# Performance work log

Measured on AMD Instinct MI355X. Metric: run time of the kernel, lower is better.

Reference implementation:

```python
import jax, jax.numpy as jnp
import numpy as np

B, C, S, HEADS, MLP = 8, 128, 32, 8, 512
EPS = 1e-5
SCALE = (C // HEADS) ** -0.5  # dim_head=16 -> 16**-0.5


def setup_inputs() -> dict:
    key = jax.random.key(0)
    ks = jax.random.split(key, 6)
    x = jax.random.normal(ks[0], (B, C, S, S, S), jnp.float32)
    qkv_w = jax.random.normal(ks[1], (3 * C, C), jnp.float32) * 0.02   # Conv3d 1x1x1, no bias
    proj_w = jax.random.normal(ks[2], (C, C), jnp.float32) * 0.02
    proj_b = jnp.zeros((C,), jnp.float32)
    ln1_w = jnp.ones((C, S, S, S), jnp.float32)
    ln1_b = jnp.zeros((C, S, S, S), jnp.float32)
    ln2_w = jnp.ones((C, S, S, S), jnp.float32)
    ln2_b = jnp.zeros((C, S, S, S), jnp.float32)
    mlp_w1 = jax.random.normal(ks[3], (MLP, C), jnp.float32) * 0.02
    mlp_b1 = jnp.zeros((MLP,), jnp.float32)
    mlp_w2 = jax.random.normal(ks[4], (C, MLP), jnp.float32) * 0.02
    mlp_b2 = jnp.zeros((C,), jnp.float32)
    return dict(x=x, qkv_w=qkv_w, proj_w=proj_w, proj_b=proj_b,
                ln1_w=ln1_w, ln1_b=ln1_b, ln2_w=ln2_w, ln2_b=ln2_b,
                mlp_w1=mlp_w1, mlp_b1=mlp_b1, mlp_w2=mlp_w2, mlp_b2=mlp_b2)


def _layernorm_full(x, w, b):
    # LayerNorm over (channel, D, H, W) per batch element, biased variance, eps=1e-5
    mu = jnp.mean(x, axis=(1, 2, 3, 4), keepdims=True)
    var = jnp.mean(jnp.square(x - mu), axis=(1, 2, 3, 4), keepdims=True)
    return (x - mu) * jax.lax.rsqrt(var + EPS) * w[None] + b[None]


def _block(x, qkv_w, proj_w, proj_b, ln1_w, ln1_b, ln2_w, ln2_b,
           mlp_w1, mlp_b1, mlp_w2, mlp_b2):
    b, c, d, h, w = x.shape
    n = d * h * w
    ch = c // HEADS
    xf = x.reshape(b, c, n)
    # 1x1x1 conv == per-voxel matmul over channels
    qkv = jnp.einsum('bcn,oc->bon', xf, qkv_w)                 # [b, 3c, n]
    q, k, v = jnp.split(qkv, 3, axis=1)
    q = q.reshape(b, HEADS, ch, n)
    k = k.reshape(b, HEADS, ch, n)
    v = v.reshape(b, HEADS, ch, n)
    # channel-channel attention: contraction over spatial tokens n
    attn = jax.nn.softmax(jnp.einsum('bhin,bhjn->bhij', q, k) * SCALE, axis=-1)
    out = jnp.einsum('bhij,bhjn->bhin', attn, v).reshape(b, c, n)
    out = jnp.einsum('bcn,oc->bon', out, proj_w) + proj_b[None, :, None]
    x1 = _layernorm_full(x + out.reshape(b, c, d, h, w), ln1_w, ln1_b)
    # MLP: conv1x1 -> exact GELU -> conv1x1
    x1f = x1.reshape(b, c, n)
    hid = jax.nn.gelu(jnp.einsum('bcn,oc->bon', x1f, mlp_w1) + mlp_b1[None, :, None],
                      approximate=False)
    m = jnp.einsum('bon,co->bcn', hid, mlp_w2) + mlp_b2[None, :, None]
    return _layernorm_full(x1 + m.reshape(b, c, d, h, w), ln2_w, ln2_b)


def reference(x, qkv_w, proj_w, proj_b, ln1_w, ln1_b, ln2_w, ln2_b,
              mlp_w1, mlp_b1, mlp_w2, mlp_b2):
    return _block(x, qkv_w, proj_w, proj_b, ln1_w, ln1_b, ln2_w, ln2_b,
                  mlp_w1, mlp_b1, mlp_w2, mlp_b2)
```

## Files before the change

kernel.cpp:

```cpp
#include <hip/hip_runtime.h>
#include <hip/hip_bf16.h>
#include <math.h>


#define N_SP 32768
typedef __hip_bfloat16 bf16;
static const size_t DS = (size_t)128 * N_SP;

typedef __attribute__((ext_vector_type(8))) short s8b;
typedef __attribute__((ext_vector_type(4))) float f4;
typedef __attribute__((ext_vector_type(4))) uint u4v;
typedef __attribute__((ext_vector_type(4))) ushort us4v;

__device__ __forceinline__ ushort f2b(float f) {
    __hip_bfloat16 h = __float2bfloat16(f);
    return *reinterpret_cast<ushort*>(&h);
}
__device__ __forceinline__ float b2f(ushort u) {
    unsigned v = ((unsigned)u) << 16;
    float f;
    __builtin_memcpy(&f, &v, 4);
    return f;
}
__device__ __forceinline__ float gelu_f(float h) {
    float u = 1.5957691216057308f * h * fmaf(0.044715f, h * h, 1.0f);
    float e = __expf(u);
    return h * (1.0f - __builtin_amdgcn_rcpf(e + 1.0f));
}
__device__ __forceinline__ int swz8(int n, int c0) {
    return n * 128 + (c0 ^ ((n & 15) << 3));
}
__device__ __forceinline__ int swz4(int n, int c0) {
    return n * 128 + (((c0 & 0x78) ^ ((n & 15) << 3)) | (c0 & 4));
}

__global__ __launch_bounds__(256) void k_transpose(const float* __restrict__ in,
                                                   float* __restrict__ out,
                                                   int R, int Ccols) {
    int idx = blockIdx.x * 256 + threadIdx.x;
    if (idx >= R * Ccols) return;
    int r = idx / Ccols, c = idx % Ccols;
    out[c * R + r] = in[idx];
}

__global__ __launch_bounds__(256) void k_cvt(const float* __restrict__ in,
                                             ushort* __restrict__ out, int n) {
    int i = blockIdx.x * 256 + threadIdx.x;
    if (i < n) out[i] = f2b(in[i]);
}

__global__ __launch_bounds__(256) void k_packln(const float* __restrict__ w,
                                                const float* __restrict__ b,
                                                uint* __restrict__ out) {
    __shared__ uint tile[64 * 128];
    const int n0 = blockIdx.x * 64;
    const int t = threadIdx.x;
    {
        const int c = t >> 1, nh = (t & 1) * 32;
        const float* wp = w + (size_t)c * N_SP + n0 + nh;
        const float* bp = b + (size_t)c * N_SP + n0 + nh;
#pragma unroll
        for (int g = 0; g < 8; ++g) {
            f4 wv = __builtin_nontemporal_load((const f4*)(wp + g * 4));
            f4 bv = __builtin_nontemporal_load((const f4*)(bp + g * 4));
            tile[(nh + g * 4 + 0) * 128 + c] = (uint)f2b(wv.x) | ((uint)f2b(bv.x) << 16);
            tile[(nh + g * 4 + 1) * 128 + c] = (uint)f2b(wv.y) | ((uint)f2b(bv.y) << 16);
            tile[(nh + g * 4 + 2) * 128 + c] = (uint)f2b(wv.z) | ((uint)f2b(bv.z) << 16);
            tile[(nh + g * 4 + 3) * 128 + c] = (uint)f2b(wv.w) | ((uint)f2b(bv.w) << 16);
        }
    }
    __syncthreads();
    uint* op = out + (size_t)n0 * 128;
#pragma unroll
    for (int g = 0; g < 8; ++g) {
        int idx = g * 256 + t;
        *(uint4*)(op + idx * 4) = *(const uint4*)&tile[idx * 4];
    }
}

__global__ __launch_bounds__(256, 4) void k_cov(const float* __restrict__ x,
                                                float* __restrict__ Gpart) {
    __shared__ ushort xs[128 * 136];
    const int kb = blockIdx.x, b = blockIdx.y;
    const int t = threadIdx.x;
    const int wave = t >> 6, lane = t & 63, q = lane >> 4, r = lane & 15;
    f4 acc[8][2];
#pragma unroll
    for (int m = 0; m < 8; ++m) { acc[m][0] = (f4){0,0,0,0}; acc[m][1] = (f4){0,0,0,0}; }
    for (int ch = 0; ch < 4; ++ch) {
        const int nbase = kb * 512 + ch * 128;
        __syncthreads();
        {
            const int nq = t & 31, cr = t >> 5;
            const float* xp = x + (size_t)b * DS + nbase + nq * 4;
#pragma unroll
            for (int half = 0; half < 2; ++half) {
                f4 xv[8];
#pragma unroll
                for (int cc = 0; cc < 8; ++cc)
                    xv[cc] = __builtin_nontemporal_load(
                        (const f4*)(xp + (size_t)(cr * 16 + half * 8 + cc) * N_SP));
#pragma unroll
                for (int cc = 0; cc < 8; ++cc) {
                    int c = cr * 16 + half * 8 + cc;
                    ushort4 pk;
                    pk.x = f2b(xv[cc].x); pk.y = f2b(xv[cc].y);
                    pk.z = f2b(xv[cc].z); pk.w = f2b(xv[cc].w);
                    *(ushort4*)&xs[c * 136 + nq * 4] = pk;
                }
            }
        }
        __syncthreads();
        for (int kk = 0; kk < 4; ++kk) {
            const int c0 = kk * 32 + q * 8;
            s8b bj0 = *(const s8b*)&xs[(wave * 32 + r) * 136 + c0];
            s8b bj1 = *(const s8b*)&xs[(wave * 32 + 16 + r) * 136 + c0];
#pragma unroll
            for (int m = 0; m < 8; ++m) {
                s8b a = *(const s8b*)&xs[(m * 16 + r) * 136 + c0];
                acc[m][0] = __builtin_amdgcn_mfma_f32_16x16x32_bf16(a, bj0, acc[m][0], 0, 0, 0);
                acc[m][1] = __builtin_amdgcn_mfma_f32_16x16x32_bf16(a, bj1, acc[m][1], 0, 0, 0);
            }
        }
    }
    float* gp = Gpart + ((size_t)b * 64 + kb) * 16384;
#pragma unroll
    for (int n2 = 0; n2 < 2; ++n2)
#pragma unroll
        for (int m = 0; m < 8; ++m)
#pragma unroll
            for (int rg = 0; rg < 4; ++rg) {
                int i = m * 16 + q * 4 + rg;
                int j = wave * 32 + n2 * 16 + r;
                gp[i * 128 + j] = acc[m][n2][rg];
            }
}

__global__ __launch_bounds__(256) void k_greduce(const float* __restrict__ Gpart,
                                                 float* __restrict__ G) {
    int tid = blockIdx.x * 256 + threadIdx.x;
    int b = tid >> 14, ij = tid & 16383;
    float s = 0.f;
#pragma unroll 8
    for (int kb = 0; kb < 64; ++kb)
        s += __builtin_nontemporal_load(&Gpart[((size_t)b * 64 + kb) * 16384 + ij]);
    G[tid] = s;
}

__global__ __launch_bounds__(256) void k_gram_small(const float* __restrict__ G,
                                                    const float* __restrict__ qkv_w,
                                                    float* __restrict__ attn) {
    __shared__ float t1[16 * 132];
    __shared__ float sg[16 * 16];
    const int bh = blockIdx.x;
    const int b = bh >> 3, h = bh & 7;
    const int t = threadIdx.x;
    {
        const int i = t >> 4, c20 = (t & 15) * 8;
        const float* wq = qkv_w + (size_t)(h * 16 + i) * 128;
        const float* Gb = G + (size_t)b * 16384;
        float a[8];
#pragma unroll
        for (int k = 0; k < 8; ++k) a[k] = 0.f;
        for (int c = 0; c < 128; ++c) {
            float w = wq[c];
            const float* grow = Gb + c * 128 + c20;
#pragma unroll
            for (int k = 0; k < 8; ++k) a[k] = fmaf(w, grow[k], a[k]);
        }
#pragma unroll
        for (int k = 0; k < 8; ++k) t1[i * 132 + c20 + k] = a[k];
    }
    __syncthreads();
    {
        const int i = t >> 4, j = t & 15;
        const float* wk = qkv_w + (size_t)(128 + h * 16 + j) * 128;
        float s = 0.f;
        for (int c2 = 0; c2 < 128; ++c2) s = fmaf(t1[i * 132 + c2], wk[c2], s);
        sg[i * 16 + j] = s * 0.25f;
    }
    __syncthreads();
    if (t < 16) {
        float mx = -1e30f;
#pragma unroll
        for (int j = 0; j < 16; ++j) mx = fmaxf(mx, sg[t * 16 + j]);
        float e[16], sum = 0.f;
#pragma unroll
        for (int j = 0; j < 16; ++j) { e[j] = expf(sg[t * 16 + j] - mx); sum += e[j]; }
        float inv = 1.0f / sum;
#pragma unroll
        for (int j = 0; j < 16; ++j)
            attn[((size_t)bh * 16 + t) * 16 + j] = e[j] * inv;
    }
}

__global__ __launch_bounds__(256, 2) void k_mfold(const float* __restrict__ attn,
                                                  const float* __restrict__ qkv_w,
                                                  const float* __restrict__ PT,
                                                  ushort* __restrict__ Mbb) {
    __shared__ float t2[128 * 128];
    const int b = blockIdx.x, t = threadIdx.x;
    {
        const int hi = t >> 1, c0 = (t & 1) * 64;
        const int h = hi >> 4;
        const float* at = attn + ((size_t)b * 128 + hi) * 16;
        float a[16];
#pragma unroll
        for (int j = 0; j < 16; ++j) a[j] = at[j];
        float sc[64];
#pragma unroll
        for (int c = 0; c < 64; ++c) sc[c] = 0.f;
        for (int j = 0; j < 16; ++j) {
            const float* wv = qkv_w + (size_t)(256 + h * 16 + j) * 128 + c0;
            float aj = a[j];
#pragma unroll
            for (int c = 0; c < 64; ++c) sc[c] = fmaf(aj, wv[c], sc[c]);
        }
#pragma unroll
        for (int c = 0; c < 64; ++c) t2[hi * 128 + c0 + c] = sc[c];
    }
    __syncthreads();
    const int c = t & 127, half = t >> 7;
    float acc[128];
#pragma unroll
    for (int o = 0; o < 128; ++o) acc[o] = 0.f;
    for (int ci = half * 64; ci < half * 64 + 64; ++ci) {
        float s = t2[ci * 128 + c];
        const float* pt = PT + ci * 128;
#pragma unroll
        for (int o = 0; o < 128; ++o) acc[o] = fmaf(pt[o], s, acc[o]);
    }
    __syncthreads();
    if (half) {
#pragma unroll
        for (int o = 0; o < 128; ++o) t2[c * 128 + o] = acc[o];
    }
    __syncthreads();
    if (!half) {
        ushort* m = Mbb + (size_t)b * 16384;
#pragma unroll
        for (int o = 0; o < 128; ++o)
            m[(size_t)o * 128 + c] = f2b(acc[o] + t2[c * 128 + o]);
    }
}

__global__ __launch_bounds__(256, 3) void k_attnproj(const float* __restrict__ x,
                                                     const ushort* __restrict__ Mbb,
                                                     const float* __restrict__ proj_b,
                                                     ushort* __restrict__ x1Tb,
                                                     float* __restrict__ st) {
    __shared__ ushort xT[128 * 136];
    const int b = blockIdx.y;
    const int n0 = blockIdx.x * 128;
    const int t = threadIdx.x;
    const int wave = t >> 6, lane = t & 63, q = lane >> 4, r = lane & 15;
    {
        const int nq = (t & 31) * 4;
        const int cg = (t >> 5) * 4;
        const float* xb = x + (size_t)b * DS + n0 + nq;
#pragma unroll
        for (int ph = 0; ph < 2; ++ph) {
            f4 xv[8];
#pragma unroll
            for (int u = 0; u < 8; ++u) {
                int c = ph * 64 + cg + (u >> 2) * 32 + (u & 3);
                xv[u] = __builtin_nontemporal_load((const f4*)(xb + (size_t)c * N_SP));
            }
#pragma unroll
            for (int u2 = 0; u2 < 2; ++u2) {
                int c0 = ph * 64 + cg + u2 * 32;
#pragma unroll
                for (int i = 0; i < 4; ++i) {
                    us4v pk = { f2b(xv[u2 * 4 + 0][i]), f2b(xv[u2 * 4 + 1][i]),
                                f2b(xv[u2 * 4 + 2][i]), f2b(xv[u2 * 4 + 3][i]) };
                    *(us4v*)&xT[(nq + i) * 136 + c0] = pk;
                }
            }
        }
    }
    const int orow = wave * 32 + r;
    s8b a[8];
    {
        const ushort* mp = Mbb + (size_t)b * 16384 + (size_t)orow * 128 + q * 8;
#pragma unroll
        for (int m = 0; m < 2; ++m)
#pragma unroll
            for (int kk = 0; kk < 4; ++kk)
                a[m * 4 + kk] = *(const s8b*)(mp + m * 16 * 128 + kk * 32);
    }
    __syncthreads();
    f4 acc[2][8];
#pragma unroll
    for (int m = 0; m < 2; ++m)
#pragma unroll
        for (int j = 0; j < 8; ++j) acc[m][j] = (f4){0,0,0,0};
#pragma unroll
    for (int kk = 0; kk < 4; ++kk) {
        const int c0 = kk * 32 + q * 8;
#pragma unroll
        for (int j = 0; j < 8; ++j) {
            s8b bx = *(const s8b*)&xT[(j * 16 + r) * 136 + c0];
            acc[0][j] = __builtin_amdgcn_mfma_f32_16x16x32_bf16(a[kk],     bx, acc[0][j], 0, 0, 0);
            acc[1][j] = __builtin_amdgcn_mfma_f32_16x16x32_bf16(a[4 + kk], bx, acc[1][j], 0, 0, 0);
        }
    }
    float s = 0.f, sq = 0.f;
    float4 pbq0 = *(const float4*)&proj_b[wave * 32 + q * 4];
    float4 pbq1 = *(const float4*)&proj_b[wave * 32 + 16 + q * 4];
#pragma unroll
    for (int j = 0; j < 8; ++j) {
        const int nn = j * 16 + r;
        ushort* obase = x1Tb + (size_t)b * DS + (size_t)(n0 + nn) * 128;
#pragma unroll
        for (int m = 0; m < 2; ++m) {
            const int o0 = wave * 32 + m * 16 + q * 4;
            const float4 pb = m ? pbq1 : pbq0;
            ushort4 xr = *(const ushort4*)&xT[nn * 136 + o0];
            float v0 = acc[m][j][0] + pb.x + b2f(xr.x);
            float v1 = acc[m][j][1] + pb.y + b2f(xr.y);
            float v2 = acc[m][j][2] + pb.z + b2f(xr.z);
            float v3 = acc[m][j][3] + pb.w + b2f(xr.w);
            us4v ov = { f2b(v0), f2b(v1), f2b(v2), f2b(v3) };
            __builtin_nontemporal_store(ov, (us4v*)(obase + o0));
            s += (v0 + v1) + (v2 + v3);
            sq = fmaf(v0, v0, sq); sq = fmaf(v1, v1, sq);
            sq = fmaf(v2, v2, sq); sq = fmaf(v3, v3, sq);
        }
    }
#pragma unroll
    for (int off = 32; off > 0; off >>= 1) {
        s += __shfl_down(s, off, 64);
        sq += __shfl_down(sq, off, 64);
    }
    if (lane == 0) {
        atomicAdd(&st[0 + b], s);
        atomicAdd(&st[8 + b], sq);
    }
}

__global__ void k_finalize(float* st, int off) {
    int b = threadIdx.x;
    if (b < 8) {
        const float invn = 1.0f / 4194304.0f;
        float mu = st[off + b] * invn;
        float var = st[off + 8 + b] * invn - mu * mu;
        st[off + 16 + b] = mu;
        st[off + 24 + b] = rsqrtf(var + 1e-5f);
    }
}

__global__ __launch_bounds__(256) void k_lnapply(const float* __restrict__ in,
                                                 const float* __restrict__ lnw,
                                                 const float* __restrict__ lnb,
                                                 const float* __restrict__ st, int off,
                                                 float* __restrict__ out) {
    size_t i4 = (size_t)blockIdx.x * 256 + threadIdx.x;
    int b = (int)(i4 >> 20);
    size_t cn = i4 * 4 - (size_t)b * 4194304;
    float mu = st[off + 16 + b], rs = st[off + 24 + b];
    const float4 xv = *(const float4*)(in + (size_t)b * DS + cn);
    const float4 wv = *(const float4*)(lnw + cn);
    const float4 bv = *(const float4*)(lnb + cn);
    float4 o;
    o.x = fmaf((xv.x - mu) * rs, wv.x, bv.x);
    o.y = fmaf((xv.y - mu) * rs, wv.y, bv.y);
    o.z = fmaf((xv.z - mu) * rs, wv.z, bv.z);
    o.w = fmaf((xv.w - mu) * rs, wv.w, bv.w);
    *(float4*)(out + (size_t)b * DS + cn) = o;
}

__global__ __launch_bounds__(256, 2) void k_mlp(const ushort* __restrict__ x1Tb,
                                                float* __restrict__ xout,
                                                const ushort* __restrict__ w1b,
                                                const float* __restrict__ b1v,
                                                const ushort* __restrict__ w2b,
                                                const float* __restrict__ b2v,
                                                const uint* __restrict__ lnwbT,
                                                float* __restrict__ st) {
    __shared__ ushort xT[128 * 128];
    __shared__ ushort hT[128 * 128];
    const int b = blockIdx.y;
    const int n0 = blockIdx.x * 128;
    const int t = threadIdx.x;
    const int wave = t >> 6, lane = t & 63, q = lane >> 4, r = lane & 15;
    const float mu = st[16 + b], rs = st[24 + b];
    {
        const int c8 = (t & 15) * 8, rb = t >> 4;
        const ushort* xb = x1Tb + (size_t)b * DS + (size_t)n0 * 128;
        const uint*  wb = lnwbT + (size_t)n0 * 128;
#pragma unroll
        for (int gb = 0; gb < 2; ++gb) {
            s8b xv[4]; u4v wv0[4], wv1[4];
#pragma unroll
            for (int u = 0; u < 4; ++u) {
                int nn = (gb * 4 + u) * 16 + rb;
                xv[u]  = __builtin_nontemporal_load((const s8b*)(xb + (size_t)nn * 128 + c8));
                wv0[u] = __builtin_nontemporal_load((const u4v*)(wb + (size_t)nn * 128 + c8));
                wv1[u] = __builtin_nontemporal_load((const u4v*)(wb + (size_t)nn * 128 + c8 + 4));
            }
#pragma unroll
            for (int u = 0; u < 4; ++u) {
                int nn = (gb * 4 + u) * 16 + rb;
                ushort4 p0, p1;
                float xe;
                xe = b2f((ushort)xv[u][0]);
                p0.x = f2b(fmaf((xe - mu) * rs, b2f((ushort)(wv0[u].x & 0xffffu)), b2f((ushort)(wv0[u].x >> 16))));
                xe = b2f((ushort)xv[u][1]);
                p0.y = f2b(fmaf((xe - mu) * rs, b2f((ushort)(wv0[u].y & 0xffffu)), b2f((ushort)(wv0[u].y >> 16))));
                xe = b2f((ushort)xv[u][2]);
                p0.z = f2b(fmaf((xe - mu) * rs, b2f((ushort)(wv0[u].z & 0xffffu)), b2f((ushort)(wv0[u].z >> 16))));
                xe = b2f((ushort)xv[u][3]);
                p0.w = f2b(fmaf((xe - mu) * rs, b2f((ushort)(wv0[u].w & 0xffffu)), b2f((ushort)(wv0[u].w >> 16))));
                xe = b2f((ushort)xv[u][4]);
                p1.x = f2b(fmaf((xe - mu) * rs, b2f((ushort)(wv1[u].x & 0xffffu)), b2f((ushort)(wv1[u].x >> 16))));
                xe = b2f((ushort)xv[u][5]);
                p1.y = f2b(fmaf((xe - mu) * rs, b2f((ushort)(wv1[u].y & 0xffffu)), b2f((ushort)(wv1[u].y >> 16))));
                xe = b2f((ushort)xv[u][6]);
                p1.z = f2b(fmaf((xe - mu) * rs, b2f((ushort)(wv1[u].z & 0xffffu)), b2f((ushort)(wv1[u].z >> 16))));
                xe = b2f((ushort)xv[u][7]);
                p1.w = f2b(fmaf((xe - mu) * rs, b2f((ushort)(wv1[u].w & 0xffffu)), b2f((ushort)(wv1[u].w >> 16))));
                *(ushort4*)&xT[swz4(nn, c8)] = p0;
                *(ushort4*)&xT[swz4(nn, c8 + 4)] = p1;
            }
        }
    }
    const int orow = wave * 32 + r;
    s8b a1[8];
    {
        const ushort* w1p = w1b + (size_t)orow * 128 + q * 8;
#pragma unroll
        for (int m = 0; m < 2; ++m)
#pragma unroll
            for (int kk = 0; kk < 4; ++kk)
                a1[m * 4 + kk] = *(const s8b*)(w1p + m * 16 * 128 + kk * 32);
    }
    __syncthreads();
    float4 b2q0 = *(const float4*)&b2v[wave * 32 + q * 4];
    float4 b2q1 = *(const float4*)&b2v[wave * 32 + 16 + q * 4];
    f4 acc2[2][8];
#pragma unroll
    for (int j = 0; j < 8; ++j) {
        acc2[0][j] = (f4){b2q0.x, b2q0.y, b2q0.z, b2q0.w};
        acc2[1][j] = (f4){b2q1.x, b2q1.y, b2q1.z, b2q1.w};
    }

    for (int os = 0; os < 4; ++os) {
        float4 b1q0 = *(const float4*)&b1v[os * 128 + wave * 32 + q * 4];
        float4 b1q1 = *(const float4*)&b1v[os * 128 + wave * 32 + 16 + q * 4];
        f4 acc1[2][8];
#pragma unroll
        for (int j = 0; j < 8; ++j) {
            acc1[0][j] = (f4){b1q0.x, b1q0.y, b1q0.z, b1q0.w};
            acc1[1][j] = (f4){b1q1.x, b1q1.y, b1q1.z, b1q1.w};
        }
#pragma unroll
        for (int kk = 0; kk < 4; ++kk) {
            const int c0 = kk * 32 + q * 8;
#pragma unroll
            for (int j = 0; j < 8; ++j) {
                s8b bx = *(const s8b*)&xT[swz8(j * 16 + r, c0)];
                acc1[0][j] = __builtin_amdgcn_mfma_f32_16x16x32_bf16(a1[kk],     bx, acc1[0][j], 0, 0, 0);
                acc1[1][j] = __builtin_amdgcn_mfma_f32_16x16x32_bf16(a1[4 + kk], bx, acc1[1][j], 0, 0, 0);
            }
        }
        s8b a2[8];
        {
            const ushort* w2p = w2b + (size_t)orow * 512 + os * 128 + q * 8;
#pragma unroll
            for (int m = 0; m < 2; ++m)
#pragma unroll
                for (int kk = 0; kk < 4; ++kk)
                    a2[m * 4 + kk] = *(const s8b*)(w2p + m * 16 * 512 + kk * 32);
        }
#pragma unroll
        for (int m = 0; m < 2; ++m) {
            const int hr0 = wave * 32 + m * 16 + q * 4;
#pragma unroll
            for (int j = 0; j < 8; ++j) {
                ushort4 pk;
                pk.x = f2b(gelu_f(acc1[m][j][0]));
                pk.y = f2b(gelu_f(acc1[m][j][1]));
                pk.z = f2b(gelu_f(acc1[m][j][2]));
                pk.w = f2b(gelu_f(acc1[m][j][3]));
                *(ushort4*)&hT[swz4(j * 16 + r, hr0)] = pk;
            }
        }
        __syncthreads();
#pragma unroll
        for (int kk = 0; kk < 4; ++kk) {
            const int c0 = kk * 32 + q * 8;
#pragma unroll
            for (int j = 0; j < 8; ++j) {
                s8b hx = *(const s8b*)&hT[swz8(j * 16 + r, c0)];
                acc2[0][j] = __builtin_amdgcn_mfma_f32_16x16x32_bf16(a2[kk],     hx, acc2[0][j], 0, 0, 0);
                acc2[1][j] = __builtin_amdgcn_mfma_f32_16x16x32_bf16(a2[4 + kk], hx, acc2[1][j], 0, 0, 0);
            }
        }
        if (os < 3) {
            const ushort* w1p = w1b + (size_t)((os + 1) * 128 + orow) * 128 + q * 8;
#pragma unroll
            for (int m = 0; m < 2; ++m)
#pragma unroll
                for (int kk = 0; kk < 4; ++kk)
                    a1[m * 4 + kk] = *(const s8b*)(w1p + m * 16 * 128 + kk * 32);
        }
        __syncthreads();
    }
    float s = 0.f, sq = 0.f;
#pragma unroll
    for (int m = 0; m < 2; ++m) {
        const int o0 = wave * 32 + m * 16 + q * 4;
#pragma unroll
        for (int j = 0; j < 8; ++j) {
            const int nn = j * 16 + r;
            ushort4 xr = *(const ushort4*)&xT[swz4(nn, o0)];
            float v0 = acc2[m][j][0] + b2f(xr.x);
            float v1 = acc2[m][j][1] + b2f(xr.y);
            float v2 = acc2[m][j][2] + b2f(xr.z);
            float v3 = acc2[m][j][3] + b2f(xr.w);
            float* op = xout + (size_t)b * DS + n0 + nn;
            op[(size_t)(o0 + 0) * N_SP] = v0;
            op[(size_t)(o0 + 1) * N_SP] = v1;
            op[(size_t)(o0 + 2) * N_SP] = v2;
            op[(size_t)(o0 + 3) * N_SP] = v3;
            s += (v0 + v1) + (v2 + v3);
            sq = fmaf(v0, v0, sq); sq = fmaf(v1, v1, sq);
            sq = fmaf(v2, v2, sq); sq = fmaf(v3, v3, sq);
        }
    }
#pragma unroll
    for (int off = 32; off > 0; off >>= 1) {
        s += __shfl_down(s, off, 64);
        sq += __shfl_down(sq, off, 64);
    }
    if (lane == 0) {
        atomicAdd(&st[32 + b], s);
        atomicAdd(&st[40 + b], sq);
    }
}

extern "C" void kernel_launch(void* const* d_in, const int* in_sizes, int n_in,
                              void* d_out, int out_size, void* d_ws, size_t ws_size,
                              hipStream_t stream) {
    const float* x      = (const float*)d_in[0];
    const float* qkv_w  = (const float*)d_in[1];
    const float* proj_w = (const float*)d_in[2];
    const float* proj_b = (const float*)d_in[3];
    const float* ln1_w  = (const float*)d_in[4];
    const float* ln1_b  = (const float*)d_in[5];
    const float* ln2_w  = (const float*)d_in[6];
    const float* ln2_b  = (const float*)d_in[7];
    const float* mlp_w1 = (const float*)d_in[8];
    const float* mlp_b1 = (const float*)d_in[9];
    const float* mlp_w2 = (const float*)d_in[10];
    const float* mlp_b2 = (const float*)d_in[11];
    float* out = (float*)d_out;

    char* wsb = (char*)d_ws;
    float*  st    = (float*)wsb;
    float*  attn  = (float*)(wsb + 256);
    float*  PT    = (float*)(wsb + 65792);
    ushort* Mbb   = (ushort*)(wsb + 131328);
    ushort* w1b   = (ushort*)(wsb + 393472);
    ushort* w2b   = (ushort*)(wsb + 524544);
    float*  G     = (float*)(wsb + 655616);
    uint*   lnwbT = (uint*)(wsb + 1179904);
    float*  Gpart = (float*)(wsb + 18874368);
    ushort* x1Tb  = (ushort*)(wsb + 18874368);

    hipMemsetAsync(st, 0, 64 * sizeof(float), stream);

    k_transpose<<<64, 256, 0, stream>>>(proj_w, PT, 128, 128);
    k_cvt<<<256, 256, 0, stream>>>(mlp_w1, w1b, 65536);
    k_cvt<<<256, 256, 0, stream>>>(mlp_w2, w2b, 65536);
    k_packln<<<512, 256, 0, stream>>>(ln1_w, ln1_b, lnwbT);

    k_cov<<<dim3(64, 8), 256, 0, stream>>>(x, Gpart);
    k_greduce<<<512, 256, 0, stream>>>(Gpart, G);
    k_gram_small<<<64, 256, 0, stream>>>(G, qkv_w, attn);
    k_mfold<<<8, 256, 0, stream>>>(attn, qkv_w, PT, Mbb);

    k_attnproj<<<dim3(256, 8), 256, 0, stream>>>(x, Mbb, proj_b, x1Tb, st);
    k_finalize<<<1, 64, 0, stream>>>(st, 0);
    k_mlp<<<dim3(256, 8), 256, 0, stream>>>(x1Tb, out, w1b, mlp_b1, w2b, mlp_b2,
                                            lnwbT, st);
    k_finalize<<<1, 64, 0, stream>>>(st, 32);
    k_lnapply<<<32768, 256, 0, stream>>>(out, ln2_w, ln2_b, st, 32, out);
}
```

Measured before the change: 958.2 us.

## Double wave count per tile in attnproj/MLP and split mfold across column blocks

The attention-projection and MLP kernels now use 512 threads per block. Each of 8 waves owns 16 output rows instead of 32, which halves the per-wave accumulator and A-fragment registers so more waves can run at once to hide latency. k_mfold is split over a 4x8 grid, each block handling 32 columns with a padded shared tile, instead of 8 blocks each doing the full 128x128 fold. The cost is that B-operand LDS reads are duplicated across twice as many waves.

Result: slower. 1.293 ms (+34.9%).

```diff
diff --git a/kernel.cpp b/kernel.cpp
--- a/kernel.cpp
+++ b/kernel.cpp
@@ -198,53 +198,47 @@
                                                   const float* __restrict__ qkv_w,
                                                   const float* __restrict__ PT,
                                                   ushort* __restrict__ Mbb) {
-    __shared__ float t2[128 * 128];
-    const int b = blockIdx.x, t = threadIdx.x;
-    {
-        const int hi = t >> 1, c0 = (t & 1) * 64;
+    __shared__ float t2[128 * 33];
+    const int c0b = blockIdx.x * 32;
+    const int b = blockIdx.y;
+    const int t = threadIdx.x;
+    {
+        const int hi = t & 127, cg2 = (t >> 7) * 16;
         const int h = hi >> 4;
         const float* at = attn + ((size_t)b * 128 + hi) * 16;
         float a[16];
 #pragma unroll
         for (int j = 0; j < 16; ++j) a[j] = at[j];
-        float sc[64];
-#pragma unroll
-        for (int c = 0; c < 64; ++c) sc[c] = 0.f;
+        float sc[16];
+#pragma unroll
+        for (int c = 0; c < 16; ++c) sc[c] = 0.f;
         for (int j = 0; j < 16; ++j) {
-            const float* wv = qkv_w + (size_t)(256 + h * 16 + j) * 128 + c0;
+            const float* wv = qkv_w + (size_t)(256 + h * 16 + j) * 128 + c0b + cg2;
             float aj = a[j];
 #pragma unroll
-            for (int c = 0; c < 64; ++c) sc[c] = fmaf(aj, wv[c], sc[c]);
-        }
-#pragma unroll
-        for (int c = 0; c < 64; ++c) t2[hi * 128 + c0 + c] = sc[c];
+            for (int c = 0; c < 16; ++c) sc[c] = fmaf(aj, wv[c], sc[c]);
+        }
+#pragma unroll
+        for (int c = 0; c < 16; ++c) t2[hi * 33 + cg2 + c] = sc[c];
     }
     __syncthreads();
-    const int c = t & 127, half = t >> 7;
-    float acc[128];
-#pragma unroll
-    for (int o = 0; o < 128; ++o) acc[o] = 0.f;
-    for (int ci = half * 64; ci < half * 64 + 64; ++ci) {
-        float s = t2[ci * 128 + c];
-        const float* pt = PT + ci * 128;
-#pragma unroll
-        for (int o = 0; o < 128; ++o) acc[o] = fmaf(pt[o], s, acc[o]);
-    }
-    __syncthreads();
-    if (half) {
-#pragma unroll
-        for (int o = 0; o < 128; ++o) t2[c * 128 + o] = acc[o];
-    }
-    __syncthreads();
-    if (!half) {
-        ushort* m = Mbb + (size_t)b * 16384;
-#pragma unroll
-        for (int o = 0; o < 128; ++o)
-            m[(size_t)o * 128 + c] = f2b(acc[o] + t2[c * 128 + o]);
-    }
-}
-
-__global__ __launch_bounds__(256, 3) void k_attnproj(const float* __restrict__ x,
+    const int cl = t & 31, og = t >> 5;
+    float acc[16];
+#pragma unroll
+    for (int o = 0; o < 16; ++o) acc[o] = 0.f;
+    for (int ci = 0; ci < 128; ++ci) {
+        float s = t2[ci * 33 + cl];
+        const float* pt = PT + ci * 128 + og * 16;
+#pragma unroll
+        for (int o = 0; o < 16; ++o) acc[o] = fmaf(pt[o], s, acc[o]);
+    }
+    ushort* m = Mbb + (size_t)b * 16384;
+#pragma unroll
+    for (int o = 0; o < 16; ++o)
+        m[(size_t)(og * 16 + o) * 128 + c0b + cl] = f2b(acc[o]);
+}
+
+__global__ __launch_bounds__(512, 4) void k_attnproj(const float* __restrict__ x,
                                                      const ushort* __restrict__ Mbb,
                                                      const float* __restrict__ proj_b,
                                                      ushort* __restrict__ x1Tb,
@@ -258,74 +252,61 @@
         const int nq = (t & 31) * 4;
         const int cg = (t >> 5) * 4;
         const float* xb = x + (size_t)b * DS + n0 + nq;
-#pragma unroll
-        for (int ph = 0; ph < 2; ++ph) {
-            f4 xv[8];
-#pragma unroll
-            for (int u = 0; u < 8; ++u) {
-                int c = ph * 64 + cg + (u >> 2) * 32 + (u & 3);
-                xv[u] = __builtin_nontemporal_load((const f4*)(xb + (size_t)c * N_SP));
+        f4 xv[8];
+#pragma unroll
+        for (int u = 0; u < 8; ++u) {
+            int c = cg + (u >> 2) * 64 + (u & 3);
+            xv[u] = __builtin_nontemporal_load((const f4*)(xb + (size_t)c * N_SP));
+        }
+#pragma unroll
+        for (int u2 = 0; u2 < 2; ++u2) {
+            int c0 = cg + u2 * 64;
+#pragma unroll
+            for (int i = 0; i < 4; ++i) {
+                us4v pk = { f2b(xv[u2 * 4 + 0][i]), f2b(xv[u2 * 4 + 1][i]),
+                            f2b(xv[u2 * 4 + 2][i]), f2b(xv[u2 * 4 + 3][i]) };
+                *(us4v*)&xT[(nq + i) * 136 + c0] = pk;
             }
-#pragma unroll
-            for (int u2 = 0; u2 < 2; ++u2) {
-                int c0 = ph * 64 + cg + u2 * 32;
-#pragma unroll
-                for (int i = 0; i < 4; ++i) {
-                    us4v pk = { f2b(xv[u2 * 4 + 0][i]), f2b(xv[u2 * 4 + 1][i]),
-                                f2b(xv[u2 * 4 + 2][i]), f2b(xv[u2 * 4 + 3][i]) };
-                    *(us4v*)&xT[(nq + i) * 136 + c0] = pk;
-                }
-            }
-        }
-    }
-    const int orow = wave * 32 + r;
-    s8b a[8];
+        }
+    }
+    const int orow = wave * 16 + r;
+    s8b a[4];
     {
         const ushort* mp = Mbb + (size_t)b * 16384 + (size_t)orow * 128 + q * 8;
 #pragma unroll
-        for (int m = 0; m < 2; ++m)
-#pragma unroll
-            for (int kk = 0; kk < 4; ++kk)
-                a[m * 4 + kk] = *(const s8b*)(mp + m * 16 * 128 + kk * 32);
+        for (int kk = 0; kk < 4; ++kk)
+            a[kk] = *(const s8b*)(mp + kk * 32);
     }
     __syncthreads();
-    f4 acc[2][8];
-#pragma unroll
-    for (int m = 0; m < 2; ++m)
-#pragma unroll
-        for (int j = 0; j < 8; ++j) acc[m][j] = (f4){0,0,0,0};
+    f4 acc[8];
+#pragma unroll
+    for (int j = 0; j < 8; ++j) acc[j] = (f4){0,0,0,0};
 #pragma unroll
     for (int kk = 0; kk < 4; ++kk) {
         const int c0 = kk * 32 + q * 8;
 #pragma unroll
         for (int j = 0; j < 8; ++j) {
             s8b bx = *(const s8b*)&xT[(j * 16 + r) * 136 + c0];
-            acc[0][j] = __builtin_amdgcn_mfma_f32_16x16x32_bf16(a[kk],     bx, acc[0][j], 0, 0, 0);
-            acc[1][j] = __builtin_amdgcn_mfma_f32_16x16x32_bf16(a[4 + kk], bx, acc[1][j], 0, 0, 0);
+            acc[j] = __builtin_amdgcn_mfma_f32_16x16x32_bf16(a[kk], bx, acc[j], 0, 0, 0);
         }
     }
     float s = 0.f, sq = 0.f;
-    float4 pbq0 = *(const float4*)&proj_b[wave * 32 + q * 4];
-    float4 pbq1 = *(const float4*)&proj_b[wave * 32 + 16 + q * 4];
+    const int o0 = wave * 16 + q * 4;
+    float4 pb = *(const float4*)&proj_b[o0];
 #pragma unroll
     for (int j = 0; j < 8; ++j) {
         const int nn = j * 16 + r;
-        ushort* obase = x1Tb + (size_t)b * DS + (size_t)(n0 + nn) * 128;
-#pragma unroll
-        for (int m = 0; m < 2; ++m) {
-            const int o0 = wave * 32 + m * 16 + q * 4;
-            const float4 pb = m ? pbq1 : pbq0;
-            ushort4 xr = *(const ushort4*)&xT[nn * 136 + o0];
-            float v0 = acc[m][j][0] + pb.x + b2f(xr.x);
-            float v1 = acc[m][j][1] + pb.y + b2f(xr.y);
-            float v2 = acc[m][j][2] + pb.z + b2f(xr.z);
-            float v3 = acc[m][j][3] + pb.w + b2f(xr.w);
-            us4v ov = { f2b(v0), f2b(v1), f2b(v2), f2b(v3) };
-            __builtin_nontemporal_store(ov, (us4v*)(obase + o0));
-            s += (v0 + v1) + (v2 + v3);
-            sq = fmaf(v0, v0, sq); sq = fmaf(v1, v1, sq);
-            sq = fmaf(v2, v2, sq); sq = fmaf(v3, v3, sq);
-        }
+        ushort4 xr = *(const ushort4*)&xT[nn * 136 + o0];
+        float v0 = acc[j][0] + pb.x + b2f(xr.x);
+        float v1 = acc[j][1] + pb.y + b2f(xr.y);
+        float v2 = acc[j][2] + pb.z + b2f(xr.z);
+        float v3 = acc[j][3] + pb.w + b2f(xr.w);
+        us4v ov = { f2b(v0), f2b(v1), f2b(v2), f2b(v3) };
+        __builtin_nontemporal_store(ov,
+            (us4v*)(x1Tb + (size_t)b * DS + (size_t)(n0 + nn) * 128 + o0));
+        s += (v0 + v1) + (v2 + v3);
+        sq = fmaf(v0, v0, sq); sq = fmaf(v1, v1, sq);
+        sq = fmaf(v2, v2, sq); sq = fmaf(v3, v3, sq);
     }
 #pragma unroll
     for (int off = 32; off > 0; off >>= 1) {
@@ -369,7 +350,7 @@
     *(float4*)(out + (size_t)b * DS + cn) = o;
 }
 
-__global__ __launch_bounds__(256, 2) void k_mlp(const ushort* __restrict__ x1Tb,
+__global__ __launch_bounds__(512, 4) void k_mlp(const ushort* __restrict__ x1Tb,
                                                 float* __restrict__ xout,
                                                 const ushort* __restrict__ w1b,
                                                 const float* __restrict__ b1v,
@@ -388,102 +369,86 @@
         const int c8 = (t & 15) * 8, rb = t >> 4;
         const ushort* xb = x1Tb + (size_t)b * DS + (size_t)n0 * 128;
         const uint*  wb = lnwbT + (size_t)n0 * 128;
-#pragma unroll
-        for (int gb = 0; gb < 2; ++gb) {
-            s8b xv[4]; u4v wv0[4], wv1[4];
-#pragma unroll
-            for (int u = 0; u < 4; ++u) {
-                int nn = (gb * 4 + u) * 16 + rb;
-                xv[u]  = __builtin_nontemporal_load((const s8b*)(xb + (size_t)nn * 128 + c8));
-                wv0[u] = __builtin_nontemporal_load((const u4v*)(wb + (size_t)nn * 128 + c8));
-                wv1[u] = __builtin_nontemporal_load((const u4v*)(wb + (size_t)nn * 128 + c8 + 4));
-            }
-#pragma unroll
-            for (int u = 0; u < 4; ++u) {
-                int nn = (gb * 4 + u) * 16 + rb;
-                ushort4 p0, p1;
-                float xe;
-                xe = b2f((ushort)xv[u][0]);
-                p0.x = f2b(fmaf((xe - mu) * rs, b2f((ushort)(wv0[u].x & 0xffffu)), b2f((ushort)(wv0[u].x >> 16))));
-                xe = b2f((ushort)xv[u][1]);
-                p0.y = f2b(fmaf((xe - mu) * rs, b2f((ushort)(wv0[u].y & 0xffffu)), b2f((ushort)(wv0[u].y >> 16))));
-                xe = b2f((ushort)xv[u][2]);
-                p0.z = f2b(fmaf((xe - mu) * rs, b2f((ushort)(wv0[u].z & 0xffffu)), b2f((ushort)(wv0[u].z >> 16))));
-                xe = b2f((ushort)xv[u][3]);
-                p0.w = f2b(fmaf((xe - mu) * rs, b2f((ushort)(wv0[u].w & 0xffffu)), b2f((ushort)(wv0[u].w >> 16))));
-                xe = b2f((ushort)xv[u][4]);
-                p1.x = f2b(fmaf((xe - mu) * rs, b2f((ushort)(wv1[u].x & 0xffffu)), b2f((ushort)(wv1[u].x >> 16))));
-                xe = b2f((ushort)xv[u][5]);
-                p1.y = f2b(fmaf((xe - mu) * rs, b2f((ushort)(wv1[u].y & 0xffffu)), b2f((ushort)(wv1[u].y >> 16))));
-                xe = b2f((ushort)xv[u][6]);
-                p1.z = f2b(fmaf((xe - mu) * rs, b2f((ushort)(wv1[u].z & 0xffffu)), b2f((ushort)(wv1[u].z >> 16))));
-                xe = b2f((ushort)xv[u][7]);
-                p1.w = f2b(fmaf((xe - mu) * rs, b2f((ushort)(wv1[u].w & 0xffffu)), b2f((ushort)(wv1[u].w >> 16))));
-                *(ushort4*)&xT[swz4(nn, c8)] = p0;
-                *(ushort4*)&xT[swz4(nn, c8 + 4)] = p1;
-            }
-        }
-    }
-    const int orow = wave * 32 + r;
-    s8b a1[8];
+        s8b xv[4]; u4v wv0[4], wv1[4];
+#pragma unroll
+        for (int u = 0; u < 4; ++u) {
+            int nn = u * 32 + rb;
+            xv[u]  = __builtin_nontemporal_load((const s8b*)(xb + (size_t)nn * 128 + c8));
+            wv0[u] = __builtin_nontemporal_load((const u4v*)(wb + (size_t)nn * 128 + c8));
+            wv1[u] = __builtin_nontemporal_load((const u4v*)(wb + (size_t)nn * 128 + c8 + 4));
+        }
+#pragma unroll
+        for (int u = 0; u < 4; ++u) {
+            int nn = u * 32 + rb;
+            ushort4 p0, p1;
+            float xe;
+            xe = b2f((ushort)xv[u][0]);
+            p0.x = f2b(fmaf((xe - mu) * rs, b2f((ushort)(wv0[u].x & 0xffffu)), b2f((ushort)(wv0[u].x >> 16))));
+            xe = b2f((ushort)xv[u][1]);
+            p0.y = f2b(fmaf((xe - mu) * rs, b2f((ushort)(wv0[u].y & 0xffffu)), b2f((ushort)(wv0[u].y >> 16))));
+            xe = b2f((ushort)xv[u][2]);
+            p0.z = f2b(fmaf((xe - mu) * rs, b2f((ushort)(wv0[u].z & 0xffffu)), b2f((ushort)(wv0[u].z >> 16))));
+            xe = b2f((ushort)xv[u][3]);
+            p0.w = f2b(fmaf((xe - mu) * rs, b2f((ushort)(wv0[u].w & 0xffffu)), b2f((ushort)(wv0[u].w >> 16))));
+            xe = b2f((ushort)xv[u][4]);
+            p1.x = f2b(fmaf((xe - mu) * rs, b2f((ushort)(wv1[u].x & 0xffffu)), b2f((ushort)(wv1[u].x >> 16))));
+            xe = b2f((ushort)xv[u][5]);
+            p1.y = f2b(fmaf((xe - mu) * rs, b2f((ushort)(wv1[u].y & 0xffffu)), b2f((ushort)(wv1[u].y >> 16))));
+            xe = b2f((ushort)xv[u][6]);
+            p1.z = f2b(fmaf((xe - mu) * rs, b2f((ushort)(wv1[u].z & 0xffffu)), b2f((ushort)(wv1[u].z >> 16))));
+            xe = b2f((ushort)xv[u][7]);
+            p1.w = f2b(fmaf((xe - mu) * rs, b2f((ushort)(wv1[u].w & 0xffffu)), b2f((ushort)(wv1[u].w >> 16))));
+            *(ushort4*)&xT[swz4(nn, c8)] = p0;
+            *(ushort4*)&xT[swz4(nn, c8 + 4)] = p1;
+        }
+    }
+    const int orow = wave * 16 + r;
+    s8b a1[4];
     {
         const ushort* w1p = w1b + (size_t)orow * 128 + q * 8;
 #pragma unroll
-        for (int m = 0; m < 2; ++m)
-#pragma unroll
-            for (int kk = 0; kk < 4; ++kk)
-                a1[m * 4 + kk] = *(const s8b*)(w1p + m * 16 * 128 + kk * 32);
+        for (int kk = 0; kk < 4; ++kk)
+            a1[kk] = *(const s8b*)(w1p + kk * 32);
     }
     __syncthreads();
-    float4 b2q0 = *(const float4*)&b2v[wave * 32 + q * 4];
-    float4 b2q1 = *(const float4*)&b2v[wave * 32 + 16 + q * 4];
-    f4 acc2[2][8];
-#pragma unroll
-    for (int j = 0; j < 8; ++j) {
-        acc2[0][j] = (f4){b2q0.x, b2q0.y, b2q0.z, b2q0.w};
-        acc2[1][j] = (f4){b2q1.x, b2q1.y, b2q1.z, b2q1.w};
-    }
+    const int o0 = wave * 16 + q * 4;
+    float4 b2q = *(const float4*)&b2v[o0];
+    f4 acc2[8];
+#pragma unroll
+    for (int j = 0; j < 8; ++j)
+        acc2[j] = (f4){b2q.x, b2q.y, b2q.z, b2q.w};
 
     for (int os = 0; os < 4; ++os) {
-        float4 b1q0 = *(const float4*)&b1v[os * 128 + wave * 32 + q * 4];
-        float4 b1q1 = *(const float4*)&b1v[os * 128 + wave * 32 + 16 + q * 4];
-        f4 acc1[2][8];
-#pragma unroll
-        for (int j = 0; j < 8; ++j) {
-            acc1[0][j] = (f4){b1q0.x, b1q0.y, b1q0.z, b1q0.w};
-            acc1[1][j] = (f4){b1q1.x, b1q1.y, b1q1.z, b1q1.w};
-        }
+        float4 b1q = *(const float4*)&b1v[os * 128 + o0];
+        f4 acc1[8];
+#pragma unroll
+        for (int j = 0; j < 8; ++j)
+            acc1[j] = (f4){b1q.x, b1q.y, b1q.z, b1q.w};
 #pragma unroll
         for (int kk = 0; kk < 4; ++kk) {
             const int c0 = kk * 32 + q * 8;
 #pragma unroll
             for (int j = 0; j < 8; ++j) {
                 s8b bx = *(const s8b*)&xT[swz8(j * 16 + r, c0)];
-                acc1[0][j] = __builtin_amdgcn_mfma_f32_16x16x32_bf16(a1[kk],     bx, acc1[0][j], 0, 0, 0);
-                acc1[1][j] = __builtin_amdgcn_mfma_f32_16x16x32_bf16(a1[4 + kk], bx, acc1[1][j], 0, 0, 0);
+                acc1[j] = __builtin_amdgcn_mfma_f32_16x16x32_bf16(a1[kk], bx, acc1[j], 0, 0, 0);
             }
         }
-        s8b a2[8];
+        s8b a2[4];
         {
             const ushort* w2p = w2b + (size_t)orow * 512 + os * 128 + q * 8;
 #pragma unroll
-            for (int m = 0; m < 2; ++m)
-#pragma unroll
-                for (int kk = 0; kk < 4; ++kk)
-                    a2[m * 4 + kk] = *(const s8b*)(w2p + m * 16 * 512 + kk * 32);
-        }
-#pragma unroll
-        for (int m = 0; m < 2; ++m) {
-            const int hr0 = wave * 32 + m * 16 + q * 4;
-#pragma unroll
-            for (int j = 0; j < 8; ++j) {
-                ushort4 pk;
-                pk.x = f2b(gelu_f(acc1[m][j][0]));
-                pk.y = f2b(gelu_f(acc1[m][j][1]));
-                pk.z = f2b(gelu_f(acc1[m][j][2]));
-                pk.w = f2b(gelu_f(acc1[m][j][3]));
-                *(ushort4*)&hT[swz4(j * 16 + r, hr0)] = pk;
-            }
+            for (int kk = 0; kk < 4; ++kk)
+                a2[kk] = *(const s8b*)(w2p + kk * 32);
+        }
+        const int hr0 = wave * 16 + q * 4;
+#pragma unroll
+        for (int j = 0; j < 8; ++j) {
+            ushort4 pk;
+            pk.x = f2b(gelu_f(acc1[j][0]));
+            pk.y = f2b(gelu_f(acc1[j][1]));
+            pk.z = f2b(gelu_f(acc1[j][2]));
+            pk.w = f2b(gelu_f(acc1[j][3]));
+            *(ushort4*)&hT[swz4(j * 16 + r, hr0)] = pk;
         }
         __syncthreads();
 #pragma unroll
@@ -492,41 +457,34 @@
 #pragma unroll
             for (int j = 0; j < 8; ++j) {
                 s8b hx = *(const s8b*)&hT[swz8(j * 16 + r, c0)];
-                acc2[0][j] = __builtin_amdgcn_mfma_f32_16x16x32_bf16(a2[kk],     hx, acc2[0][j], 0, 0, 0);
-                acc2[1][j] = __builtin_amdgcn_mfma_f32_16x16x32_bf16(a2[4 + kk], hx, acc2[1][j], 0, 0, 0);
+                acc2[j] = __builtin_amdgcn_mfma_f32_16x16x32_bf16(a2[kk], hx, acc2[j], 0, 0, 0);
             }
         }
         if (os < 3) {
             const ushort* w1p = w1b + (size_t)((os + 1) * 128 + orow) * 128 + q * 8;
 #pragma unroll
-            for (int m = 0; m < 2; ++m)
-#pragma unroll
-                for (int kk = 0; kk < 4; ++kk)
-                    a1[m * 4 + kk] = *(const s8b*)(w1p + m * 16 * 128 + kk * 32);
+            for (int kk = 0; kk < 4; ++kk)
+                a1[kk] = *(const s8b*)(w1p + kk * 32);
         }
         __syncthreads();
     }
     float s = 0.f, sq = 0.f;
 #pragma unroll
-    for (int m = 0; m < 2; ++m) {
-        const int o0 = wave * 32 + m * 16 + q * 4;
-#pragma unroll
-        for (int j = 0; j < 8; ++j) {
-            const int nn = j * 16 + r;
-            ushort4 xr = *(const ushort4*)&xT[swz4(nn, o0)];
-            float v0 = acc2[m][j][0] + b2f(xr.x);
-            float v1 = acc2[m][j][1] + b2f(xr.y);
-            float v2 = acc2[m][j][2] + b2f(xr.z);
-            float v3 = acc2[m][j][3] + b2f(xr.w);
-            float* op = xout + (size_t)b * DS + n0 + nn;
-            op[(size_t)(o0 + 0) * N_SP] = v0;
-            op[(size_t)(o0 + 1) * N_SP] = v1;
-            op[(size_t)(o0 + 2) * N_SP] = v2;
-            op[(size_t)(o0 + 3) * N_SP] = v3;
-            s += (v0 + v1) + (v2 + v3);
-            sq = fmaf(v0, v0, sq); sq = fmaf(v1, v1, sq);
-            sq = fmaf(v2, v2, sq); sq = fmaf(v3, v3, sq);
-        }
+    for (int j = 0; j < 8; ++j) {
+        const int nn = j * 16 + r;
+        ushort4 xr = *(const ushort4*)&xT[swz4(nn, o0)];
+        float v0 = acc2[j][0] + b2f(xr.x);
+        float v1 = acc2[j][1] + b2f(xr.y);
+        float v2 = acc2[j][2] + b2f(xr.z);
+        float v3 = acc2[j][3] + b2f(xr.w);
+        float* op = xout + (size_t)b * DS + n0 + nn;
+        op[(size_t)(o0 + 0) * N_SP] = v0;
+        op[(size_t)(o0 + 1) * N_SP] = v1;
+        op[(size_t)(o0 + 2) * N_SP] = v2;
+        op[(size_t)(o0 + 3) * N_SP] = v3;
+        s += (v0 + v1) + (v2 + v3);
+        sq = fmaf(v0, v0, sq); sq = fmaf(v1, v1, sq);
+        sq = fmaf(v2, v2, sq); sq = fmaf(v3, v3, sq);
     }
 #pragma unroll
     for (int off = 32; off > 0; off >>= 1) {
@@ -578,11 +536,11 @@
     k_cov<<<dim3(64, 8), 256, 0, stream>>>(x, Gpart);
     k_greduce<<<512, 256, 0, stream>>>(Gpart, G);
     k_gram_small<<<64, 256, 0, stream>>>(G, qkv_w, attn);
-    k_mfold<<<8, 256, 0, stream>>>(attn, qkv_w, PT, Mbb);
-
-    k_attnproj<<<dim3(256, 8), 256, 0, stream>>>(x, Mbb, proj_b, x1Tb, st);
+    k_mfold<<<dim3(4, 8), 256, 0, stream>>>(attn, qkv_w, PT, Mbb);
+
+    k_attnproj<<<dim3(256, 8), 512, 0, stream>>>(x, Mbb, proj_b, x1Tb, st);
     k_finalize<<<1, 64, 0, stream>>>(st, 0);
-    k_mlp<<<dim3(256, 8), 256, 0, stream>>>(x1Tb, out, w1b, mlp_b1, w2b, mlp_b2,
+    k_mlp<<<dim3(256, 8), 512, 0, stream>>>(x1Tb, out, w1b, mlp_b1, w2b, mlp_b2,
                                             lnwbT, st);
     k_finalize<<<1, 64, 0, stream>>>(st, 32);
     k_lnapply<<<32768, 256, 0, stream>>>(out, ln2_w, ln2_b, st, 32, out);
```

## Merge prep kernels, drop finalize launches, parallelize mfold across column tiles

Applied to the files above, without the earlier changes.

Combines the transpose, two weight conversions and LN-weight packing into one k_prep launch. It removes both k_finalize launches by computing mean and rstd inline from the raw sums in the consuming kernels. It also splits k_mfold into 4 column tiles per batch, which cuts per-thread register arrays and the shared buffer, raises the grid from 8 to 32 blocks, and removes the half-sum reduction. The aim is to cut launch overhead and the serial tail of small kernels. The cost is redundant stats math per thread.

Result: faster. 887.9 us (-7.3%).

```diff
diff --git a/kernel.cpp b/kernel.cpp
--- a/kernel.cpp
+++ b/kernel.cpp
@@ -27,6 +27,13 @@
     float e = __expf(u);
     return h * (1.0f - __builtin_amdgcn_rcpf(e + 1.0f));
 }
+__device__ __forceinline__ void ln_stats(const float* st, int off, int b,
+                                         float& mu, float& rs) {
+    const float invn = 1.0f / 4194304.0f;
+    mu = st[off + b] * invn;
+    float var = st[off + 8 + b] * invn - mu * mu;
+    rs = rsqrtf(var + 1e-5f);
+}
 __device__ __forceinline__ int swz8(int n, int c0) {
     return n * 128 + (c0 ^ ((n & 15) << 3));
 }
@@ -34,47 +41,50 @@
     return n * 128 + (((c0 & 0x78) ^ ((n & 15) << 3)) | (c0 & 4));
 }
 
-__global__ __launch_bounds__(256) void k_transpose(const float* __restrict__ in,
-                                                   float* __restrict__ out,
-                                                   int R, int Ccols) {
-    int idx = blockIdx.x * 256 + threadIdx.x;
-    if (idx >= R * Ccols) return;
-    int r = idx / Ccols, c = idx % Ccols;
-    out[c * R + r] = in[idx];
-}
-
-__global__ __launch_bounds__(256) void k_cvt(const float* __restrict__ in,
-                                             ushort* __restrict__ out, int n) {
-    int i = blockIdx.x * 256 + threadIdx.x;
-    if (i < n) out[i] = f2b(in[i]);
-}
-
-__global__ __launch_bounds__(256) void k_packln(const float* __restrict__ w,
-                                                const float* __restrict__ b,
-                                                uint* __restrict__ out) {
+__global__ __launch_bounds__(256) void k_prep(const float* __restrict__ proj_w,
+                                              float* __restrict__ PT,
+                                              const float* __restrict__ mlp_w1,
+                                              ushort* __restrict__ w1b,
+                                              const float* __restrict__ mlp_w2,
+                                              ushort* __restrict__ w2b,
+                                              const float* __restrict__ ln1w,
+                                              const float* __restrict__ ln1b,
+                                              uint* __restrict__ lnwbT) {
     __shared__ uint tile[64 * 128];
-    const int n0 = blockIdx.x * 64;
-    const int t = threadIdx.x;
-    {
-        const int c = t >> 1, nh = (t & 1) * 32;
-        const float* wp = w + (size_t)c * N_SP + n0 + nh;
-        const float* bp = b + (size_t)c * N_SP + n0 + nh;
+    const int bx = blockIdx.x, t = threadIdx.x;
+    if (bx < 512) {
+        const int n0 = bx * 64;
+        {
+            const int c = t >> 1, nh = (t & 1) * 32;
+            const float* wp = ln1w + (size_t)c * N_SP + n0 + nh;
+            const float* bp = ln1b + (size_t)c * N_SP + n0 + nh;
+#pragma unroll
+            for (int g = 0; g < 8; ++g) {
+                f4 wv = __builtin_nontemporal_load((const f4*)(wp + g * 4));
+                f4 bv = __builtin_nontemporal_load((const f4*)(bp + g * 4));
+                tile[(nh + g * 4 + 0) * 128 + c] = (uint)f2b(wv.x) | ((uint)f2b(bv.x) << 16);
+                tile[(nh + g * 4 + 1) * 128 + c] = (uint)f2b(wv.y) | ((uint)f2b(bv.y) << 16);
+                tile[(nh + g * 4 + 2) * 128 + c] = (uint)f2b(wv.z) | ((uint)f2b(bv.z) << 16);
+                tile[(nh + g * 4 + 3) * 128 + c] = (uint)f2b(wv.w) | ((uint)f2b(bv.w) << 16);
+            }
+        }
+        __syncthreads();
+        uint* op = lnwbT + (size_t)n0 * 128;
 #pragma unroll
         for (int g = 0; g < 8; ++g) {
-            f4 wv = __builtin_nontemporal_load((const f4*)(wp + g * 4));
-            f4 bv = __builtin_nontemporal_load((const f4*)(bp + g * 4));
-            tile[(nh + g * 4 + 0) * 128 + c] = (uint)f2b(wv.x) | ((uint)f2b(bv.x) << 16);
-            tile[(nh + g * 4 + 1) * 128 + c] = (uint)f2b(wv.y) | ((uint)f2b(bv.y) << 16);
-            tile[(nh + g * 4 + 2) * 128 + c] = (uint)f2b(wv.z) | ((uint)f2b(bv.z) << 16);
-            tile[(nh + g * 4 + 3) * 128 + c] = (uint)f2b(wv.w) | ((uint)f2b(bv.w) << 16);
-        }
-    }
-    __syncthreads();
-    uint* op = out + (size_t)n0 * 128;
-#pragma unroll
-    for (int g = 0; g < 8; ++g) {
-        int idx = g * 256 + t;
-        *(uint4*)(op + idx * 4) = *(const uint4*)&tile[idx * 4];
+            int idx = g * 256 + t;
+            *(uint4*)(op + idx * 4) = *(const uint4*)&tile[idx * 4];
+        }
+    } else if (bx < 576) {
+        int idx = (bx - 512) * 256 + t;
+        int r = idx >> 7, c = idx & 127;
+        PT[c * 128 + r] = proj_w[idx];
+    } else if (bx < 832) {
+        int i = (bx - 576) * 256 + t;
+        w1b[i] = f2b(mlp_w1[i]);
+    } else {
+        int i = (bx - 832) * 256 + t;
+        w2b[i] = f2b(mlp_w2[i]);
     }
 }
 
@@ -198,50 +208,44 @@
                                                   const float* __restrict__ qkv_w,
                                                   const float* __restrict__ PT,
                                                   ushort* __restrict__ Mbb) {
-    __shared__ float t2[128 * 128];
-    const int b = blockIdx.x, t = threadIdx.x;
-    {
-        const int hi = t >> 1, c0 = (t & 1) * 64;
+    __shared__ float t2[128 * 33];
+    const int c0b = blockIdx.x * 32;
+    const int b = blockIdx.y;
+    const int t = threadIdx.x;
+    {
+        const int hi = t & 127, cg2 = (t >> 7) * 16;
         const int h = hi >> 4;
         const float* at = attn + ((size_t)b * 128 + hi) * 16;
         float a[16];
 #pragma unroll
         for (int j = 0; j < 16; ++j) a[j] = at[j];
-        float sc[64];
-#pragma unroll
-        for (int c = 0; c < 64; ++c) sc[c] = 0.f;
+        float sc[16];
+#pragma unroll
+        for (int c = 0; c < 16; ++c) sc[c] = 0.f;
         for (int j = 0; j < 16; ++j) {
-            const float* wv = qkv_w + (size_t)(256 + h * 16 + j) * 128 + c0;
+            const float* wv = qkv_w + (size_t)(256 + h * 16 + j) * 128 + c0b + cg2;
             float aj = a[j];
 #pragma unroll
-            for (int c = 0; c < 64; ++c) sc[c] = fmaf(aj, wv[c], sc[c]);
-        }
-#pragma unroll
-        for (int c = 0; c < 64; ++c) t2[hi * 128 + c0 + c] = sc[c];
+            for (int c = 0; c < 16; ++c) sc[c] = fmaf(aj, wv[c], sc[c]);
+        }
+#pragma unroll
+        for (int c = 0; c < 16; ++c) t2[hi * 33 + cg2 + c] = sc[c];
     }
     __syncthreads();
-    const int c = t & 127, half = t >> 7;
-    float acc[128];
-#pragma unroll
-    for (int o = 0; o < 128; ++o) acc[o] = 0.f;
-    for (int ci = half * 64; ci < half * 64 + 64; ++ci) {
-        float s = t2[ci * 128 + c];
-        const float* pt = PT + ci * 128;
-#pragma unroll
-        for (int o = 0; o < 128; ++o) acc[o] = fmaf(pt[o], s, acc[o]);
-    }
-    __syncthreads();
-    if (half) {
-#pragma unroll
-        for (int o = 0; o < 128; ++o) t2[c * 128 + o] = acc[o];
-    }
-    __syncthreads();
-    if (!half) {
-        ushort* m = Mbb + (size_t)b * 16384;
-#pragma unroll
-        for (int o = 0; o < 128; ++o)
-            m[(size_t)o * 128 + c] = f2b(acc[o] + t2[c * 128 + o]);
-    }
+    const int cl = t & 31, og = t >> 5;
+    float acc[16];
+#pragma unroll
+    for (int o = 0; o < 16; ++o) acc[o] = 0.f;
+    for (int ci = 0; ci < 128; ++ci) {
+        float s = t2[ci * 33 + cl];
+        const float* pt = PT + ci * 128 + og * 16;
+#pragma unroll
+        for (int o = 0; o < 16; ++o) acc[o] = fmaf(pt[o], s, acc[o]);
+    }
+    ushort* m = Mbb + (size_t)b * 16384;
+#pragma unroll
+    for (int o = 0; o < 16; ++o)
+        m[(size_t)(og * 16 + o) * 128 + c0b + cl] = f2b(acc[o]);
 }
 
 __global__ __launch_bounds__(256, 3) void k_attnproj(const float* __restrict__ x,
@@ -338,26 +342,16 @@
     }
 }
 
-__global__ void k_finalize(float* st, int off) {
-    int b = threadIdx.x;
-    if (b < 8) {
-        const float invn = 1.0f / 4194304.0f;
-        float mu = st[off + b] * invn;
-        float var = st[off + 8 + b] * invn - mu * mu;
-        st[off + 16 + b] = mu;
-        st[off + 24 + b] = rsqrtf(var + 1e-5f);
-    }
-}
-
 __global__ __launch_bounds__(256) void k_lnapply(const float* __restrict__ in,
                                                  const float* __restrict__ lnw,
                                                  const float* __restrict__ lnb,
-                                                 const float* __restrict__ st, int off,
+                                                 const float* __restrict__ st,
                                                  float* __restrict__ out) {
     size_t i4 = (size_t)blockIdx.x * 256 + threadIdx.x;
     int b = (int)(i4 >> 20);
     size_t cn = i4 * 4 - (size_t)b * 4194304;
-    float mu = st[off + 16 + b], rs = st[off + 24 + b];
+    float mu, rs;
+    ln_stats(st, 32, b, mu, rs);
     const float4 xv = *(const float4*)(in + (size_t)b * DS + cn);
     const float4 wv = *(const float4*)(lnw + cn);
     const float4 bv = *(const float4*)(lnb + cn);
@@ -383,7 +377,8 @@
     const int n0 = blockIdx.x * 128;
     const int t = threadIdx.x;
     const int wave = t >> 6, lane = t & 63, q = lane >> 4, r = lane & 15;
-    const float mu = st[16 + b], rs = st[24 + b];
+    float mu, rs;
+    ln_stats(st, 0, b, mu, rs);
     {
         const int c8 = (t & 15) * 8, rb = t >> 4;
         const ushort* xb = x1Tb + (size_t)b * DS + (size_t)n0 * 128;
@@ -570,20 +565,16 @@
 
     hipMemsetAsync(st, 0, 64 * sizeof(float), stream);
 
-    k_transpose<<<64, 256, 0, stream>>>(proj_w, PT, 128, 128);
-    k_cvt<<<256, 256, 0, stream>>>(mlp_w1, w1b, 65536);
-    k_cvt<<<256, 256, 0, stream>>>(mlp_w2, w2b, 65536);
-    k_packln<<<512, 256, 0, stream>>>(ln1_w, ln1_b, lnwbT);
+    k_prep<<<1088, 256, 0, stream>>>(proj_w, PT, mlp_w1, w1b, mlp_w2, w2b,
+                                     ln1_w, ln1_b, lnwbT);
 
     k_cov<<<dim3(64, 8), 256, 0, stream>>>(x, Gpart);
     k_greduce<<<512, 256, 0, stream>>>(Gpart, G);
     k_gram_small<<<64, 256, 0, stream>>>(G, qkv_w, attn);
-    k_mfold<<<8, 256, 0, stream>>>(attn, qkv_w, PT, Mbb);
+    k_mfold<<<dim3(4, 8), 256, 0, stream>>>(attn, qkv_w, PT, Mbb);
 
     k_attnproj<<<dim3(256, 8), 256, 0, stream>>>(x, Mbb, proj_b, x1Tb, st);
-    k_finalize<<<1, 64, 0, stream>>>(st, 0);
     k_mlp<<<dim3(256, 8), 256, 0, stream>>>(x1Tb, out, w1b, mlp_b1, w2b, mlp_b2,
                                             lnwbT, st);
-    k_finalize<<<1, 64, 0, stream>>>(st, 32);
-    k_lnapply<<<32768, 256, 0, stream>>>(out, ln2_w, ln2_b, st, 32, out);
-}
+    k_lnapply<<<32768, 256, 0, stream>>>(out, ln2_w, ln2_b, st, out);
+}
```
